# Kernel tuning notes

Hardware: AMD Instinct MI355X
Metric: run time of the kernel (lower is better)

Reference implementation:

```python
import jax, jax.numpy as jnp
import numpy as np

B, DIM1, DIM2, HID, HEADS, H, W, OUT = 2, 256, 512, 256, 8, 48, 48, 256
HD = HID // HEADS  # 32
SCALE = HD ** -0.5


def conv1x1(x, Wt, b):
    # 1x1 Conv2d == per-pixel linear over channels
    return jnp.einsum('oc,bchw->bohw', Wt, x) + b[None, :, None, None]


def setup_inputs() -> dict:
    key = jax.random.key(0)
    ks = jax.random.split(key, 18)
    s1, s2, sh = 1.0 / np.sqrt(DIM1), 1.0 / np.sqrt(DIM2), 1.0 / np.sqrt(HID)
    f32 = jnp.float32
    return {
        'modal1_feat': jax.random.normal(ks[0], (B, DIM1, H, W), f32),
        'modal2_feat': jax.random.normal(ks[1], (B, DIM2, H, W), f32),
        'Wq1': jax.random.normal(ks[2], (HID, DIM1), f32) * s1,
        'bq1': jax.random.normal(ks[3], (HID,), f32) * 0.01,
        'Wk1': jax.random.normal(ks[4], (HID, DIM1), f32) * s1,
        'bk1': jax.random.normal(ks[5], (HID,), f32) * 0.01,
        'Wv1': jax.random.normal(ks[6], (HID, DIM1), f32) * s1,
        'bv1': jax.random.normal(ks[7], (HID,), f32) * 0.01,
        'Wq2': jax.random.normal(ks[8], (HID, DIM2), f32) * s2,
        'bq2': jax.random.normal(ks[9], (HID,), f32) * 0.01,
        'Wk2': jax.random.normal(ks[10], (HID, DIM2), f32) * s2,
        'bk2': jax.random.normal(ks[11], (HID,), f32) * 0.01,
        'Wv2': jax.random.normal(ks[12], (HID, DIM2), f32) * s2,
        'bv2': jax.random.normal(ks[13], (HID,), f32) * 0.01,
        'Wo1': jax.random.normal(ks[14], (OUT, HID), f32) * sh,
        'bo1': jax.random.normal(ks[15], (OUT,), f32) * 0.01,
        'Wo2': jax.random.normal(ks[16], (OUT, HID), f32) * sh,
        'bo2': jax.random.normal(ks[17], (OUT,), f32) * 0.01,
    }


def reference(modal1_feat, modal2_feat, Wq1, bq1, Wk1, bk1, Wv1, bv1,
              Wq2, bq2, Wk2, bk2, Wv2, bv2, Wo1, bo1, Wo2, bo2):
    Bn, _, H1, W1 = modal1_feat.shape
    _, _, H2, W2 = modal2_feat.shape
    N1, N2 = H1 * W1, H2 * W2

    # projections, reshaped to heads; q/v -> [B,h,N,d], k -> [B,h,d,N]
    q1 = conv1x1(modal1_feat, Wq1, bq1).reshape(Bn, HEADS, HD, N1).transpose(0, 1, 3, 2)
    k1 = conv1x1(modal1_feat, Wk1, bk1).reshape(Bn, HEADS, HD, N1)
    v1 = conv1x1(modal1_feat, Wv1, bv1).reshape(Bn, HEADS, HD, N1).transpose(0, 1, 3, 2)
    q2 = conv1x1(modal2_feat, Wq2, bq2).reshape(Bn, HEADS, HD, N2).transpose(0, 1, 3, 2)
    k2 = conv1x1(modal2_feat, Wk2, bk2).reshape(Bn, HEADS, HD, N2)
    v2 = conv1x1(modal2_feat, Wv2, bv2).reshape(Bn, HEADS, HD, N2).transpose(0, 1, 3, 2)

    # bidirectional cross attention (dropout is identity in eval / p used here is 0)
    attn_1to2 = jax.nn.softmax(jnp.einsum('bhnd,bhdm->bhnm', q1, k2) * SCALE, axis=-1)
    attn_2to1 = jax.nn.softmax(jnp.einsum('bhmd,bhdn->bhmn', q2, k1) * SCALE, axis=-1)

    out1 = jnp.einsum('bhnm,bhmd->bhnd', attn_1to2, v2)  # [B,h,N1,d]
    out1 = out1.transpose(0, 1, 3, 2).reshape(Bn, HID, H1, W1)
    out2 = jnp.einsum('bhmn,bhnd->bhmd', attn_2to1, v1)  # [B,h,N2,d]
    out2 = out2.transpose(0, 1, 3, 2).reshape(Bn, HID, H2, W2)

    output1 = conv1x1(out1, Wo1, bo1)
    output2 = conv1x1(out2, Wo2, bo2)
    return (output1, output2)
```

## Files before the change

kernel.cpp:

```cpp
#include <hip/hip_runtime.h>
#include <hip/hip_bf16.h>

#define BI 2
#define NPOS 2304
#define HIDC 256
#define NH 8
#define HDIM 32
#define QSCALE (0.17677669529663687f * 1.4426950408889634f)

typedef __attribute__((ext_vector_type(8))) short short8;
typedef __attribute__((ext_vector_type(4))) short short4v;
typedef __attribute__((ext_vector_type(4))) float f32x4;
typedef __attribute__((ext_vector_type(4))) float float4v;
typedef __attribute__((ext_vector_type(2))) unsigned uint2v;

__device__ inline short f2bf(float f) {
  union { float f; unsigned u; } v; v.f = f;
  unsigned u = v.u;
  unsigned r = (u + 0x7FFFu + ((u >> 16) & 1u)) >> 16;
  return (short)r;
}

__device__ inline float bf2f(short s) {
  union { unsigned u; float f; } v;
  v.u = ((unsigned)(unsigned short)s) << 16;
  return v.f;
}

__device__ inline float exp2_asm(float x) {
  float r; asm("v_exp_f32 %0, %1" : "=v"(r) : "v"(x)); return r;
}

__device__ inline unsigned pkbf(float a, float b) {
  __hip_bfloat162 h = __float22bfloat162_rn(make_float2(a, b));
  union { __hip_bfloat162 h; unsigned u; } cv; cv.h = h;
  return cv.u;
}

__global__ __launch_bounds__(256) void convert_x(const float* X1, const float* X2,
                                                 short* X1t, short* X2t) {
  int nb = blockIdx.x, y = blockIdx.y;
  const float* X; short* Xt; int C, cb;
  if (y < 8) {
    int b = y >> 2; cb = y & 3; C = 256;
    X = X1 + (size_t)b * 256 * NPOS; Xt = X1t + (size_t)b * NPOS * 256;
  } else {
    int y2 = y - 8; int b = y2 >> 3; cb = y2 & 7; C = 512;
    X = X2 + (size_t)b * 512 * NPOS; Xt = X2t + (size_t)b * NPOS * 512;
  }
  const int c0 = cb * 64, n0 = nb * 64;
  __shared__ short T[64][68];
  const int tid = threadIdx.x;
  const int col4 = (tid & 15) * 4, rowb = tid >> 4;
#pragma unroll
  for (int p = 0; p < 4; p++) {
    int row = p * 16 + rowb;
    float4v v = *(const float4v*)(X + (size_t)(c0 + row) * NPOS + n0 + col4);
    T[col4 + 0][row] = f2bf(v[0]);
    T[col4 + 1][row] = f2bf(v[1]);
    T[col4 + 2][row] = f2bf(v[2]);
    T[col4 + 3][row] = f2bf(v[3]);
  }
  __syncthreads();
#pragma unroll
  for (int p = 0; p < 2; p++) {
    int n = p * 32 + (tid >> 3), c8 = (tid & 7) * 8;
    short8 s = *(const short8*)&T[n][c8];
    *(short8*)(Xt + (size_t)(n0 + n) * C + c0 + c8) = s;
  }
}

struct CvtWArgs {
  const float* src[8];
  short* dst[8];
  int nelem[8];
  float scale[8];
};

__global__ __launch_bounds__(256) void convert_w(CvtWArgs A) {
  const int seg = blockIdx.y;
  const int idx = (blockIdx.x * 256 + threadIdx.x) * 4;
  if (idx >= A.nelem[seg]) return;
  const float sc = A.scale[seg];
  const float4v v = *(const float4v*)(A.src[seg] + idx);
  short4v s;
  s[0] = f2bf(v[0] * sc); s[1] = f2bf(v[1] * sc);
  s[2] = f2bf(v[2] * sc); s[3] = f2bf(v[3] * sc);
  *(short4v*)(A.dst[seg] + idx) = s;
}

__global__ __launch_bounds__(256) void proj_gemm(
    const short* Wc1, const short* Wc2, const short* X1t, const short* X2t,
    const float* bq1, const float* bk1, const float* bv1,
    const float* bq2, const float* bk2, const float* bv2,
    short* Q1t, short* K1t, short* V1, short* Q2t, short* K2t, short* V2) {
  const int nblk = blockIdx.x;
  const int mblk = blockIdx.y;
  const int z = blockIdx.z;
  const int b = z >> 1, modal = z & 1;
  const int K = modal ? 512 : 256;
  const short* Wp = modal ? Wc2 : Wc1;
  const short* Xp = (modal ? X2t : X1t) + (size_t)b * NPOS * K;
  const int m0 = mblk * 64, n0 = nblk * 128;
  const int seg = mblk >> 2;

  __shared__ __attribute__((aligned(16))) short Al[64][72];
  __shared__ __attribute__((aligned(16))) short Bl[128][72];

  const int tid = threadIdx.x;
  const int lane = tid & 63;
  const int w = tid >> 6;
  const int q = lane & 15, g = lane >> 4;
  const int srow = tid >> 3, scol = (tid & 7) * 8;

  short8 ra[2], rb[4];
  auto loadt = [&](int kt) {
    ra[0] = *(const short8*)(Wp + (size_t)(m0 + srow) * K + kt + scol);
    ra[1] = *(const short8*)(Wp + (size_t)(m0 + 32 + srow) * K + kt + scol);
#pragma unroll
    for (int u = 0; u < 4; u++)
      rb[u] = *(const short8*)(Xp + (size_t)(n0 + u * 32 + srow) * K + kt + scol);
  };

  loadt(0);
  f32x4 acc[4][2];
#pragma unroll
  for (int i = 0; i < 4; i++)
#pragma unroll
    for (int j = 0; j < 2; j++)
      acc[i][j] = (f32x4){0.f, 0.f, 0.f, 0.f};

  const int NT = K / 64;
  for (int t = 0; t < NT; t++) {
    *(short8*)&Al[srow][scol] = ra[0];
    *(short8*)&Al[32 + srow][scol] = ra[1];
#pragma unroll
    for (int u = 0; u < 4; u++)
      *(short8*)&Bl[u * 32 + srow][scol] = rb[u];
    __syncthreads();
    if (t + 1 < NT) loadt((t + 1) * 64);
#pragma unroll
    for (int kk = 0; kk < 2; kk++) {
      short8 af[4], bfj[2];
#pragma unroll
      for (int i = 0; i < 4; i++)
        af[i] = *(const short8*)&Al[i * 16 + q][kk * 32 + g * 8];
#pragma unroll
      for (int j = 0; j < 2; j++)
        bfj[j] = *(const short8*)&Bl[w * 32 + j * 16 + q][kk * 32 + g * 8];
#pragma unroll
      for (int i = 0; i < 4; i++)
#pragma unroll
        for (int j = 0; j < 2; j++)
          acc[i][j] = __builtin_amdgcn_mfma_f32_16x16x32_bf16(af[i], bfj[j], acc[i][j], 0, 0, 0);
    }
    __syncthreads();
  }

  const float* bp = (seg == 0) ? (modal ? bq2 : bq1)
                  : (seg == 1) ? (modal ? bk2 : bk1)
                               : (modal ? bv2 : bv1);
  const float bscale = (seg == 0) ? (float)QSCALE : 1.0f;

  if (seg < 2) {
    short* outp = (seg == 0) ? (modal ? Q2t : Q1t) : (modal ? K2t : K1t);
#pragma unroll
    for (int i = 0; i < 4; i++) {
      int c0 = (m0 & 255) + i * 16 + g * 4;
      int h = c0 >> 5, d0 = c0 & 31;
      short* op = outp + (size_t)(b * NH + h) * NPOS * HDIM;
      float bb[4];
#pragma unroll
      for (int r = 0; r < 4; r++) bb[r] = bp[c0 + r] * bscale;
#pragma unroll
      for (int j = 0; j < 2; j++) {
        int n = n0 + w * 32 + j * 16 + q;
        short4v s;
#pragma unroll
        for (int r = 0; r < 4; r++) s[r] = f2bf(acc[i][j][r] + bb[r]);
        *(short4v*)&op[(size_t)n * HDIM + d0] = s;
      }
    }
  } else {
    short* outp = (modal ? V2 : V1) + (size_t)b * HIDC * NPOS;
#pragma unroll
    for (int i = 0; i < 4; i++) {
      int c0 = (m0 & 255) + i * 16 + g * 4;
#pragma unroll
      for (int j = 0; j < 2; j++) {
        int n = n0 + w * 32 + j * 16 + q;
#pragma unroll
        for (int r = 0; r < 4; r++)
          outp[(size_t)(c0 + r) * NPOS + n] = f2bf(acc[i][j][r] + bp[c0 + r]);
      }
    }
  }
}

__global__ __launch_bounds__(256) void attn_kernel(
    const short* Q1t, const short* K1t, const short* V1,
    const short* Q2t, const short* K2t, const short* V2,
    short* Opart, float* Lpart) {
  const int id = blockIdx.x;
  const int nid = (id & 7) * 216 + (id >> 3);
  const int sub = nid % 54;
  const int ks = sub % 3;
  const int wt = sub / 3;
  const int zh = nid / 54;
  const int h = zh & 7;
  const int z = zh >> 3;
  const int b = z >> 1, dir = z & 1;

  const short* Qp = (dir ? Q2t : Q1t) + (size_t)(b * NH + h) * NPOS * HDIM;
  const short* Kp = (dir ? K1t : K2t) + (size_t)(b * NH + h) * NPOS * HDIM;
  const short* Vp = (dir ? V1 : V2) + (size_t)b * HIDC * NPOS + (size_t)h * HDIM * NPOS;

  __shared__ __attribute__((aligned(16))) short Kl[2][64][40];
  __shared__ __attribute__((aligned(16))) short Vl[2][32][72];

  const int tid = threadIdx.x;
  const int lane = tid & 63;
  const int q = lane & 15, g = lane >> 4;
  const int w = tid >> 6;
  const int q0a = wt * 128 + w * 16;
  const int q0b = q0a + 64;
  const int k0 = ks * 768;

  const short8 qfa = *(const short8*)(Qp + (size_t)(q0a + q) * HDIM + g * 8);
  const short8 qfb = *(const short8*)(Qp + (size_t)(q0b + q) * HDIM + g * 8);

  const int krow = tid >> 2, kcol = (tid & 3) * 8;
  const int vrow = tid >> 3, vcol = (tid & 7) * 8;
  const short* Vrow = Vp + (size_t)vrow * NPOS;

  {
    short8 sk = *(const short8*)(Kp + k0 * 32 + tid * 8);
    short8 sv = *(const short8*)(Vrow + k0 + vcol);
    *(short8*)&Kl[0][krow][kcol] = sk;
    *(short8*)&Vl[0][vrow][vcol] = sv;
  }
  __syncthreads();

  short8 ones;
#pragma unroll
  for (int i = 0; i < 8; i++) ones[i] = (short)0x3F80;

  const f32x4 mC = {-32.f, -32.f, -32.f, -32.f};
  const f32x4 fz = {0.f, 0.f, 0.f, 0.f};
  f32x4 accA0 = fz, accA1 = fz, acc2A = fz;
  f32x4 accB0 = fz, accB1 = fz, acc2B = fz;
  int cur = 0;

  for (int t = 0; t < 12; t++) {
    const int ktn = k0 + ((t < 11) ? (t + 1) * 64 : 0);
    short8 sk = *(const short8*)(Kp + ktn * 32 + tid * 8);
    short8 sv = *(const short8*)(Vrow + ktn + vcol);

    short8 kfr[4];
#pragma unroll
    for (int f = 0; f < 4; f++)
      kfr[f] = *(const short8*)&Kl[cur][f * 16 + q][g * 8];

    short8 va[2][2];
#pragma unroll
    for (int dc = 0; dc < 2; dc++)
#pragma unroll
      for (int hf = 0; hf < 2; hf++) {
        union { short4v h4[2]; short8 s; } u8;
        u8.h4[0] = *(const short4v*)&Vl[cur][dc * 16 + q][hf * 32 + g * 4];
        u8.h4[1] = *(const short4v*)&Vl[cur][dc * 16 + q][hf * 32 + 16 + g * 4];
        va[dc][hf] = u8.s;
      }

    {
      f32x4 sT[4];
#pragma unroll
      for (int f = 0; f < 4; f++)
        sT[f] = __builtin_amdgcn_mfma_f32_16x16x32_bf16(kfr[f], qfa, mC, 0, 0, 0);
#pragma unroll
      for (int f = 0; f < 4; f++)
#pragma unroll
        for (int r = 0; r < 4; r++)
          sT[f][r] = exp2_asm(sT[f][r]);
      union { unsigned u[4]; short8 s; } pb0, pb1;
      pb0.u[0] = pkbf(sT[0][0], sT[0][1]); pb0.u[1] = pkbf(sT[0][2], sT[0][3]);
      pb0.u[2] = pkbf(sT[1][0], sT[1][1]); pb0.u[3] = pkbf(sT[1][2], sT[1][3]);
      pb1.u[0] = pkbf(sT[2][0], sT[2][1]); pb1.u[1] = pkbf(sT[2][2], sT[2][3]);
      pb1.u[2] = pkbf(sT[3][0], sT[3][1]); pb1.u[3] = pkbf(sT[3][2], sT[3][3]);
      accA0 = __builtin_amdgcn_mfma_f32_16x16x32_bf16(va[0][0], pb0.s, accA0, 0, 0, 0);
      accA1 = __builtin_amdgcn_mfma_f32_16x16x32_bf16(va[1][0], pb0.s, accA1, 0, 0, 0);
      acc2A = __builtin_amdgcn_mfma_f32_16x16x32_bf16(ones, pb0.s, acc2A, 0, 0, 0);
      accA0 = __builtin_amdgcn_mfma_f32_16x16x32_bf16(va[0][1], pb1.s, accA0, 0, 0, 0);
      accA1 = __builtin_amdgcn_mfma_f32_16x16x32_bf16(va[1][1], pb1.s, accA1, 0, 0, 0);
      acc2A = __builtin_amdgcn_mfma_f32_16x16x32_bf16(ones, pb1.s, acc2A, 0, 0, 0);
    }
    {
      f32x4 sT[4];
#pragma unroll
      for (int f = 0; f < 4; f++)
        sT[f] = __builtin_amdgcn_mfma_f32_16x16x32_bf16(kfr[f], qfb, mC, 0, 0, 0);
#pragma unroll
      for (int f = 0; f < 4; f++)
#pragma unroll
        for (int r = 0; r < 4; r++)
          sT[f][r] = exp2_asm(sT[f][r]);
      union { unsigned u[4]; short8 s; } pb0, pb1;
      pb0.u[0] = pkbf(sT[0][0], sT[0][1]); pb0.u[1] = pkbf(sT[0][2], sT[0][3]);
      pb0.u[2] = pkbf(sT[1][0], sT[1][1]); pb0.u[3] = pkbf(sT[1][2], sT[1][3]);
      pb1.u[0] = pkbf(sT[2][0], sT[2][1]); pb1.u[1] = pkbf(sT[2][2], sT[2][3]);
      pb1.u[2] = pkbf(sT[3][0], sT[3][1]); pb1.u[3] = pkbf(sT[3][2], sT[3][3]);
      accB0 = __builtin_amdgcn_mfma_f32_16x16x32_bf16(va[0][0], pb0.s, accB0, 0, 0, 0);
      accB1 = __builtin_amdgcn_mfma_f32_16x16x32_bf16(va[1][0], pb0.s, accB1, 0, 0, 0);
      acc2B = __builtin_amdgcn_mfma_f32_16x16x32_bf16(ones, pb0.s, acc2B, 0, 0, 0);
      accB0 = __builtin_amdgcn_mfma_f32_16x16x32_bf16(va[0][1], pb1.s, accB0, 0, 0, 0);
      accB1 = __builtin_amdgcn_mfma_f32_16x16x32_bf16(va[1][1], pb1.s, accB1, 0, 0, 0);
      acc2B = __builtin_amdgcn_mfma_f32_16x16x32_bf16(ones, pb1.s, acc2B, 0, 0, 0);
    }

    *(short8*)&Kl[cur ^ 1][krow][kcol] = sk;
    *(short8*)&Vl[cur ^ 1][vrow][vcol] = sv;
    __syncthreads();
    cur ^= 1;
  }

  const float lrA = acc2A[0];
  const float lrB = acc2B[0];

  const size_t PH = (size_t)32 * 32 * NPOS;
  short* Pp = Opart + (size_t)ks * PH + (size_t)zh * 32 * NPOS;
#pragma unroll
  for (int r = 0; r < 4; r++) {
    Pp[(size_t)(g * 4 + r) * NPOS + q0a + q] = f2bf(accA0[r]);
    Pp[(size_t)(16 + g * 4 + r) * NPOS + q0a + q] = f2bf(accA1[r]);
    Pp[(size_t)(g * 4 + r) * NPOS + q0b + q] = f2bf(accB0[r]);
    Pp[(size_t)(16 + g * 4 + r) * NPOS + q0b + q] = f2bf(accB1[r]);
  }
  if (g == 0) {
    float* Lp = Lpart + (size_t)ks * (32 * NPOS) + (size_t)zh * NPOS;
    Lp[q0a + q] = lrA;
    Lp[q0b + q] = lrB;
  }
}

__global__ __launch_bounds__(256) void merge_kernel(
    const short* Opart, const float* Lpart, short* On1, short* On2) {
  const int nt = blockIdx.x;
  const int zh = blockIdx.y;
  const int z = zh >> 3, h = zh & 7;
  const int b = z >> 1, dir = z & 1;
  const int n0 = nt * 64;
  const size_t PH = (size_t)32 * 32 * NPOS;
  const short* P0 = Opart + (size_t)zh * 32 * NPOS;
  const short* P1 = P0 + PH;
  const short* P2 = P0 + 2 * PH;
  const float* L0 = Lpart + (size_t)zh * NPOS;
  const float* L1 = L0 + (size_t)32 * NPOS;
  const float* L2 = L0 + (size_t)64 * NPOS;
  short* On = (dir ? On2 : On1) + (size_t)b * NPOS * HIDC;

  __shared__ float rl[64];
  __shared__ short T[64][36];

  const int tid = threadIdx.x;
  if (tid < 64) rl[tid] = 1.0f / (L0[n0 + tid] + L1[n0 + tid] + L2[n0 + tid]);
  __syncthreads();

  const int d = tid >> 3, nc = (tid & 7) * 8;
  short8 a = *(const short8*)(P0 + (size_t)d * NPOS + n0 + nc);
  short8 c = *(const short8*)(P1 + (size_t)d * NPOS + n0 + nc);
  short8 e = *(const short8*)(P2 + (size_t)d * NPOS + n0 + nc);
#pragma unroll
  for (int j = 0; j < 8; j++)
    T[nc + j][d] = f2bf((bf2f(a[j]) + bf2f(c[j]) + bf2f(e[j])) * rl[nc + j]);
  __syncthreads();

  const int n = tid >> 2, c8 = (tid & 3) * 8;
  short8 o = *(const short8*)&T[n][c8];
  *(short8*)(On + (size_t)(n0 + n) * HIDC + h * HDIM + c8) = o;
}

__global__ __launch_bounds__(256) void outproj_kernel(
    const short* Wo1b, const short* Wo2b, const float* bo1, const float* bo2,
    const short* On1, const short* On2, float* out) {
  const int nblk = blockIdx.x;
  const int mblk = blockIdx.y;
  const int z = blockIdx.z;
  const int dir = z >> 1, b = z & 1;
  const short* Wp = dir ? Wo2b : Wo1b;
  const float* bp = dir ? bo2 : bo1;
  const short* Xp = (dir ? On2 : On1) + (size_t)b * NPOS * HIDC;
  float* op = out + (size_t)dir * BI * HIDC * NPOS + (size_t)b * HIDC * NPOS;
  const int m0 = mblk * 64, n0 = nblk * 128;

  __shared__ __attribute__((aligned(16))) short Al[64][72];
  __shared__ __attribute__((aligned(16))) short Bl[128][72];

  const int tid = threadIdx.x;
  const int lane = tid & 63;
  const int w = tid >> 6;
  const int q = lane & 15, g = lane >> 4;
  const int srow = tid >> 3, scol = (tid & 7) * 8;

  short8 ra[2], rb[4];
  auto loadt = [&](int kt) {
    ra[0] = *(const short8*)(Wp + (size_t)(m0 + srow) * HIDC + kt + scol);
    ra[1] = *(const short8*)(Wp + (size_t)(m0 + 32 + srow) * HIDC + kt + scol);
#pragma unroll
    for (int u = 0; u < 4; u++)
      rb[u] = *(const short8*)(Xp + (size_t)(n0 + u * 32 + srow) * HIDC + kt + scol);
  };

  loadt(0);
  f32x4 acc[4][2];
#pragma unroll
  for (int i = 0; i < 4; i++)
#pragma unroll
    for (int j = 0; j < 2; j++)
      acc[i][j] = (f32x4){0.f, 0.f, 0.f, 0.f};

  for (int t = 0; t < 4; t++) {
    *(short8*)&Al[srow][scol] = ra[0];
    *(short8*)&Al[32 + srow][scol] = ra[1];
#pragma unroll
    for (int u = 0; u < 4; u++)
      *(short8*)&Bl[u * 32 + srow][scol] = rb[u];
    __syncthreads();
    if (t + 1 < 4) loadt((t + 1) * 64);
#pragma unroll
    for (int kk = 0; kk < 2; kk++) {
      short8 af[4], bfj[2];
#pragma unroll
      for (int i = 0; i < 4; i++)
        af[i] = *(const short8*)&Al[i * 16 + q][kk * 32 + g * 8];
#pragma unroll
      for (int j = 0; j < 2; j++)
        bfj[j] = *(const short8*)&Bl[w * 32 + j * 16 + q][kk * 32 + g * 8];
#pragma unroll
      for (int i = 0; i < 4; i++)
#pragma unroll
        for (int j = 0; j < 2; j++)
          acc[i][j] = __builtin_amdgcn_mfma_f32_16x16x32_bf16(af[i], bfj[j], acc[i][j], 0, 0, 0);
    }
    __syncthreads();
  }

#pragma unroll
  for (int i = 0; i < 4; i++) {
    int c0 = m0 + i * 16 + g * 4;
#pragma unroll
    for (int r = 0; r < 4; r++) {
      float bb = bp[c0 + r];
#pragma unroll
      for (int j = 0; j < 2; j++) {
        int n = n0 + w * 32 + j * 16 + q;
        op[(size_t)(c0 + r) * NPOS + n] = acc[i][j][r] + bb;
      }
    }
  }
}

extern "C" void kernel_launch(void* const* d_in, const int* in_sizes, int n_in,
                              void* d_out, int out_size, void* d_ws, size_t ws_size,
                              hipStream_t stream) {
  const float* m1 = (const float*)d_in[0];
  const float* m2 = (const float*)d_in[1];

  const size_t SZ = (size_t)BI * HIDC * NPOS;
  short* ws = (short*)d_ws;
  short* Q1t = ws + 0 * SZ;
  short* K1t = ws + 1 * SZ;
  short* V1  = ws + 2 * SZ;
  short* Q2t = ws + 3 * SZ;
  short* K2t = ws + 4 * SZ;
  short* V2  = ws + 5 * SZ;
  short* X1t = ws + 6 * SZ;
  short* X2t = ws + 7 * SZ;
  short* Opart = ws + 6 * SZ;
  float* Lpart = (float*)(ws + 12 * SZ);
  short* On1 = ws + 0 * SZ;
  short* On2 = ws + 1 * SZ;
  short* Wc1 = ws + 12 * SZ + 442368;
  short* Wc2 = Wc1 + 768 * 256;
  short* Wo1b = Wc2 + 768 * 512;
  short* Wo2b = Wo1b + 256 * 256;

  hipLaunchKernelGGL(convert_x, dim3(36, 24), dim3(256), 0, stream, m1, m2, X1t, X2t);

  CvtWArgs CW;
  CW.src[0] = (const float*)d_in[2];  CW.dst[0] = Wc1;          CW.nelem[0] = 65536;  CW.scale[0] = (float)QSCALE;
  CW.src[1] = (const float*)d_in[4];  CW.dst[1] = Wc1 + 65536;  CW.nelem[1] = 65536;  CW.scale[1] = 1.f;
  CW.src[2] = (const float*)d_in[6];  CW.dst[2] = Wc1 + 131072; CW.nelem[2] = 65536;  CW.scale[2] = 1.f;
  CW.src[3] = (const float*)d_in[8];  CW.dst[3] = Wc2;          CW.nelem[3] = 131072; CW.scale[3] = (float)QSCALE;
  CW.src[4] = (const float*)d_in[10]; CW.dst[4] = Wc2 + 131072; CW.nelem[4] = 131072; CW.scale[4] = 1.f;
  CW.src[5] = (const float*)d_in[12]; CW.dst[5] = Wc2 + 262144; CW.nelem[5] = 131072; CW.scale[5] = 1.f;
  CW.src[6] = (const float*)d_in[14]; CW.dst[6] = Wo1b;         CW.nelem[6] = 65536;  CW.scale[6] = 1.f;
  CW.src[7] = (const float*)d_in[16]; CW.dst[7] = Wo2b;         CW.nelem[7] = 65536;  CW.scale[7] = 1.f;
  hipLaunchKernelGGL(convert_w, dim3(128, 8), dim3(256), 0, stream, CW);

  hipLaunchKernelGGL(proj_gemm, dim3(18, 12, 4), dim3(256), 0, stream,
                     Wc1, Wc2, X1t, X2t,
                     (const float*)d_in[3], (const float*)d_in[5], (const float*)d_in[7],
                     (const float*)d_in[9], (const float*)d_in[11], (const float*)d_in[13],
                     Q1t, K1t, V1, Q2t, K2t, V2);

  hipLaunchKernelGGL(attn_kernel, dim3(1728), dim3(256), 0, stream,
                     Q1t, K1t, V1, Q2t, K2t, V2, Opart, Lpart);

  hipLaunchKernelGGL(merge_kernel, dim3(36, 32), dim3(256), 0, stream,
                     Opart, Lpart, On1, On2);

  hipLaunchKernelGGL(outproj_kernel, dim3(18, 4, 4), dim3(256), 0, stream,
                     Wo1b, Wo2b, (const float*)d_in[15], (const float*)d_in[17],
                     On1, On2, (float*)d_out);
}
```

Baseline: 84.75 us.

## Fuse split-K attention merge into output projection and store partials position-major

```diff
diff --git a/kernel.cpp b/kernel.cpp
--- a/kernel.cpp
+++ b/kernel.cpp
@@ -323,77 +323,43 @@
     cur ^= 1;
   }
 
-  const float lrA = acc2A[0];
-  const float lrB = acc2B[0];
-
-  const size_t PH = (size_t)32 * 32 * NPOS;
-  short* Pp = Opart + (size_t)ks * PH + (size_t)zh * 32 * NPOS;
+  const size_t PH = (size_t)32 * NPOS * 32;
+  short* Pp = Opart + (size_t)ks * PH + (size_t)zh * NPOS * 32;
+  short4v sA0, sA1, sB0, sB1;
 #pragma unroll
   for (int r = 0; r < 4; r++) {
-    Pp[(size_t)(g * 4 + r) * NPOS + q0a + q] = f2bf(accA0[r]);
-    Pp[(size_t)(16 + g * 4 + r) * NPOS + q0a + q] = f2bf(accA1[r]);
-    Pp[(size_t)(g * 4 + r) * NPOS + q0b + q] = f2bf(accB0[r]);
-    Pp[(size_t)(16 + g * 4 + r) * NPOS + q0b + q] = f2bf(accB1[r]);
-  }
+    sA0[r] = f2bf(accA0[r]); sA1[r] = f2bf(accA1[r]);
+    sB0[r] = f2bf(accB0[r]); sB1[r] = f2bf(accB1[r]);
+  }
+  *(short4v*)&Pp[(size_t)(q0a + q) * 32 + g * 4] = sA0;
+  *(short4v*)&Pp[(size_t)(q0a + q) * 32 + 16 + g * 4] = sA1;
+  *(short4v*)&Pp[(size_t)(q0b + q) * 32 + g * 4] = sB0;
+  *(short4v*)&Pp[(size_t)(q0b + q) * 32 + 16 + g * 4] = sB1;
   if (g == 0) {
     float* Lp = Lpart + (size_t)ks * (32 * NPOS) + (size_t)zh * NPOS;
-    Lp[q0a + q] = lrA;
-    Lp[q0b + q] = lrB;
-  }
-}
-
-__global__ __launch_bounds__(256) void merge_kernel(
-    const short* Opart, const float* Lpart, short* On1, short* On2) {
-  const int nt = blockIdx.x;
-  const int zh = blockIdx.y;
-  const int z = zh >> 3, h = zh & 7;
-  const int b = z >> 1, dir = z & 1;
-  const int n0 = nt * 64;
-  const size_t PH = (size_t)32 * 32 * NPOS;
-  const short* P0 = Opart + (size_t)zh * 32 * NPOS;
-  const short* P1 = P0 + PH;
-  const short* P2 = P0 + 2 * PH;
-  const float* L0 = Lpart + (size_t)zh * NPOS;
-  const float* L1 = L0 + (size_t)32 * NPOS;
-  const float* L2 = L0 + (size_t)64 * NPOS;
-  short* On = (dir ? On2 : On1) + (size_t)b * NPOS * HIDC;
-
-  __shared__ float rl[64];
-  __shared__ short T[64][36];
-
-  const int tid = threadIdx.x;
-  if (tid < 64) rl[tid] = 1.0f / (L0[n0 + tid] + L1[n0 + tid] + L2[n0 + tid]);
-  __syncthreads();
-
-  const int d = tid >> 3, nc = (tid & 7) * 8;
-  short8 a = *(const short8*)(P0 + (size_t)d * NPOS + n0 + nc);
-  short8 c = *(const short8*)(P1 + (size_t)d * NPOS + n0 + nc);
-  short8 e = *(const short8*)(P2 + (size_t)d * NPOS + n0 + nc);
-#pragma unroll
-  for (int j = 0; j < 8; j++)
-    T[nc + j][d] = f2bf((bf2f(a[j]) + bf2f(c[j]) + bf2f(e[j])) * rl[nc + j]);
-  __syncthreads();
-
-  const int n = tid >> 2, c8 = (tid & 3) * 8;
-  short8 o = *(const short8*)&T[n][c8];
-  *(short8*)(On + (size_t)(n0 + n) * HIDC + h * HDIM + c8) = o;
+    Lp[q0a + q] = acc2A[0];
+    Lp[q0b + q] = acc2B[0];
+  }
 }
 
 __global__ __launch_bounds__(256) void outproj_kernel(
     const short* Wo1b, const short* Wo2b, const float* bo1, const float* bo2,
-    const short* On1, const short* On2, float* out) {
+    const short* Opart, const float* Lpart, float* out) {
   const int nblk = blockIdx.x;
   const int mblk = blockIdx.y;
   const int z = blockIdx.z;
   const int dir = z >> 1, b = z & 1;
+  const int zatt = b * 2 + dir;
   const short* Wp = dir ? Wo2b : Wo1b;
   const float* bp = dir ? bo2 : bo1;
-  const short* Xp = (dir ? On2 : On1) + (size_t)b * NPOS * HIDC;
   float* op = out + (size_t)dir * BI * HIDC * NPOS + (size_t)b * HIDC * NPOS;
   const int m0 = mblk * 64, n0 = nblk * 128;
+  const size_t PH = (size_t)32 * NPOS * 32;
+  const size_t LH = (size_t)32 * NPOS;
 
   __shared__ __attribute__((aligned(16))) short Al[64][72];
   __shared__ __attribute__((aligned(16))) short Bl[128][72];
+  __shared__ float rl[8][128];
 
   const int tid = threadIdx.x;
   const int lane = tid & 63;
@@ -401,13 +367,29 @@
   const int q = lane & 15, g = lane >> 4;
   const int srow = tid >> 3, scol = (tid & 7) * 8;
 
-  short8 ra[2], rb[4];
+  for (int idx = tid; idx < 1024; idx += 256) {
+    const int hh = idx >> 7, npr = idx & 127;
+    const float* Lb = Lpart + (size_t)(zatt * 8 + hh) * NPOS + n0 + npr;
+    rl[hh][npr] = 1.0f / (Lb[0] + Lb[LH] + Lb[2 * LH]);
+  }
+  __syncthreads();
+
+  short8 ra[2], rb[4][3];
+  int hcur = 0;
   auto loadt = [&](int kt) {
     ra[0] = *(const short8*)(Wp + (size_t)(m0 + srow) * HIDC + kt + scol);
     ra[1] = *(const short8*)(Wp + (size_t)(m0 + 32 + srow) * HIDC + kt + scol);
-#pragma unroll
-    for (int u = 0; u < 4; u++)
-      rb[u] = *(const short8*)(Xp + (size_t)(n0 + u * 32 + srow) * HIDC + kt + scol);
+    const int c = kt + scol;
+    hcur = c >> 5;
+    const int d0 = c & 31;
+    const short* Bp = Opart + (size_t)(zatt * 8 + hcur) * NPOS * 32 + d0;
+#pragma unroll
+    for (int u = 0; u < 4; u++) {
+      const size_t off = (size_t)(n0 + u * 32 + srow) * 32;
+#pragma unroll
+      for (int s = 0; s < 3; s++)
+        rb[u][s] = *(const short8*)(Bp + (size_t)s * PH + off);
+    }
   };
 
   loadt(0);
@@ -422,8 +404,14 @@
     *(short8*)&Al[srow][scol] = ra[0];
     *(short8*)&Al[32 + srow][scol] = ra[1];
 #pragma unroll
-    for (int u = 0; u < 4; u++)
-      *(short8*)&Bl[u * 32 + srow][scol] = rb[u];
+    for (int u = 0; u < 4; u++) {
+      const float rv = rl[hcur][u * 32 + srow];
+      short8 m;
+#pragma unroll
+      for (int j = 0; j < 8; j++)
+        m[j] = f2bf((bf2f(rb[u][0][j]) + bf2f(rb[u][1][j]) + bf2f(rb[u][2][j])) * rv);
+      *(short8*)&Bl[u * 32 + srow][scol] = m;
+    }
     __syncthreads();
     if (t + 1 < 4) loadt((t + 1) * 64);
 #pragma unroll
@@ -477,8 +465,6 @@
   short* X2t = ws + 7 * SZ;
   short* Opart = ws + 6 * SZ;
   float* Lpart = (float*)(ws + 12 * SZ);
-  short* On1 = ws + 0 * SZ;
-  short* On2 = ws + 1 * SZ;
   short* Wc1 = ws + 12 * SZ + 442368;
   short* Wc2 = Wc1 + 768 * 256;
   short* Wo1b = Wc2 + 768 * 512;
@@ -506,10 +492,7 @@
   hipLaunchKernelGGL(attn_kernel, dim3(1728), dim3(256), 0, stream,
                      Q1t, K1t, V1, Q2t, K2t, V2, Opart, Lpart);
 
-  hipLaunchKernelGGL(merge_kernel, dim3(36, 32), dim3(256), 0, stream,
-                     Opart, Lpart, On1, On2);
-
   hipLaunchKernelGGL(outproj_kernel, dim3(18, 4, 4), dim3(256), 0, stream,
                      Wo1b, Wo2b, (const float*)d_in[15], (const float*)d_in[17],
-                     On1, On2, (float*)d_out);
-}
+                     Opart, Lpart, (float*)d_out);
+}
```

Measured after the change: 87.76 us. 3.6% more time.
